# Optimization experiments

Measured on AMD Instinct MI355X. Metric: run time of the kernel, lower is better.

The kernel has to match this reference:

```python
import jax, jax.numpy as jnp
import numpy as np

B, L, D = 4, 2048, 1024
H = 16
HD = D // H  # head_dim = 64
BASE = 10000.0


def rope_cos_sin(seq_len, head_dim, dtype=jnp.float32):
    inv_freq = 1.0 / (BASE ** (jnp.arange(0, head_dim, 2, dtype=jnp.float32) / head_dim))
    t = jnp.arange(seq_len, dtype=jnp.float32)
    freqs = jnp.outer(t, inv_freq)  # [L, HD/2]
    return jnp.cos(freqs).astype(dtype), jnp.sin(freqs).astype(dtype)


def apply_rope(x, cos, sin):
    # x: [B, H, L, HD]; cos/sin: [L, HD/2]
    x1 = x[..., ::2]
    x2 = x[..., 1::2]
    c = cos[None, None, :, :]
    s = sin[None, None, :, :]
    # NOTE: original concatenates halves (does not re-interleave)
    return jnp.concatenate([x1 * c - x2 * s, x1 * s + x2 * c], axis=-1)


def setup_inputs() -> dict:
    key = jax.random.key(0)
    k1, k2, k3 = jax.random.split(key, 3)
    x = jax.random.normal(k1, (B, L, D), dtype=jnp.float32)
    W_qkv = jax.random.normal(k2, (3 * D, D), dtype=jnp.float32) * (D ** -0.5)
    W_proj = jax.random.normal(k3, (D, D), dtype=jnp.float32) * (D ** -0.5)
    return {"x": x, "W_qkv": W_qkv, "W_proj": W_proj}


def reference(x, W_qkv, W_proj):
    b, l, d = x.shape
    scale = HD ** -0.5
    qkv = jnp.einsum('bld,ed->ble', x, W_qkv)            # [B, L, 3D]
    qkv = qkv.reshape(b, l, 3, H, HD)
    q, k, v = (jnp.transpose(qkv[:, :, i], (0, 2, 1, 3)) for i in range(3))  # [B,H,L,HD]
    cos, sin = rope_cos_sin(l, HD, x.dtype)
    q = apply_rope(q, cos, sin)
    k = apply_rope(k, cos, sin)
    attn = jnp.einsum('bhqd,bhkd->bhqk', q, k) * scale   # [B,H,L,L]
    attn = jax.nn.softmax(attn, axis=-1)
    out = jnp.einsum('bhqk,bhkd->bhqd', attn, v)         # [B,H,L,HD]
    out = jnp.transpose(out, (0, 2, 1, 3)).reshape(b, l, d)
    return jnp.einsum('bld,ed->ble', out, W_proj)
```

## Files before the change

### kernel.cpp

```cpp
#include <hip/hip_runtime.h>
#include <hip/hip_bf16.h>

typedef unsigned short u16;
typedef unsigned int u32;
typedef __attribute__((ext_vector_type(8))) short bf16x8;
typedef __attribute__((ext_vector_type(4))) float f32x4;

#define NL 2048
#define NH 16

__device__ __forceinline__ float bf2f(u16 v) {
    union { float f; unsigned u; } x; x.u = ((unsigned)v) << 16; return x.f;
}
__device__ __forceinline__ u16 f2bf(float f) {
    union { __hip_bfloat16 h; u16 u; } x; x.h = __float2bfloat16(f); return x.u;
}
__device__ __forceinline__ u32 pk2(float a, float b) {
    union { float f; u32 u; } x, y; x.f = a; y.f = b;
    return ((x.u + 0x8000u) >> 16) | ((y.u + 0x8000u) & 0xffff0000u);
}
__device__ __forceinline__ u32 pkt(float lo, float hi) {
    union { float f; u32 u; } x, y; x.f = lo; y.f = hi;
    return __builtin_amdgcn_perm(y.u, x.u, 0x07060302u);
}
#if __has_builtin(__builtin_amdgcn_exp2f)
#define EXP2F(x) __builtin_amdgcn_exp2f(x)
#else
#define EXP2F(x) __expf((x) * 0.69314718056f)
#endif

__device__ __forceinline__ void gload_lds16(const u16* g, u16* l) {
    __builtin_amdgcn_global_load_lds(
        (__attribute__((address_space(1))) void*)(g),
        (__attribute__((address_space(3))) void*)(l), 16, 0, 0);
}

__global__ __launch_bounds__(256) void cast_all_k(const float* __restrict__ x,
                                                  const float* __restrict__ wq,
                                                  const float* __restrict__ wp,
                                                  u16* __restrict__ xo,
                                                  u16* __restrict__ wqo,
                                                  u16* __restrict__ wpo) {
    int i = blockIdx.x * 256 + threadIdx.x;
    const float* src; u16* dst; int off;
    if (i < 2097152)      { src = x;  dst = xo;  off = i; }
    else if (i < 2883584) { src = wq; dst = wqo; off = i - 2097152; }
    else                  { src = wp; dst = wpo; off = i - 2883584; }
    float4 v = *(const float4*)&src[(size_t)off * 4];
    u16 tmp[4] = {f2bf(v.x), f2bf(v.y), f2bf(v.z), f2bf(v.w)};
    *(ushort4*)&dst[(size_t)off * 4] = *(ushort4*)tmp;
}

__global__ __launch_bounds__(256) void rope_table_k(float* __restrict__ cosT,
                                                    float* __restrict__ sinT) {
    int idx = blockIdx.x * 256 + threadIdx.x;
    int l = idx >> 5, i = idx & 31;
    float invf = exp2f(-(float)i * 0.41524101186092029f);
    float ang = (float)l * invf;
    cosT[idx] = cosf(ang);
    sinT[idx] = sinf(ang);
}

template <typename OutT>
__global__ __launch_bounds__(256) void gemm_bt(const u16* __restrict__ A,
                                               const u16* __restrict__ Bm,
                                               OutT* __restrict__ C,
                                               int M, int N, int K) {
    __shared__ u16 As[128][64];
    __shared__ u16 Bs[128][64];
    const int t = threadIdx.x;
    const int lane = t & 63, wave = t >> 6;
    const int quad = lane >> 4, lrow = lane & 15;
    const int wr = wave >> 1, wc = wave & 1;
    const size_t m0 = (size_t)blockIdx.y * 128, n0 = (size_t)blockIdx.x * 128;

    const int srow = wave * 32 + (lane >> 3);
    const int scg  = (lane & 7) ^ (lane >> 3);

    f32x4 acc[4][4];
#pragma unroll
    for (int i = 0; i < 4; ++i)
#pragma unroll
        for (int j = 0; j < 4; ++j) acc[i][j] = (f32x4)0.0f;

    for (int k0 = 0; k0 < K; k0 += 64) {
#pragma unroll
        for (int j = 0; j < 4; ++j) {
            gload_lds16(&A[(m0 + srow + j * 8) * K + k0 + scg * 8],
                        &As[wave * 32 + j * 8][0]);
            gload_lds16(&Bm[(n0 + srow + j * 8) * K + k0 + scg * 8],
                        &Bs[wave * 32 + j * 8][0]);
        }
        __syncthreads();
#pragma unroll
        for (int ks = 0; ks < 2; ++ks) {
            bf16x8 av[4], bv[4];
#pragma unroll
            for (int i = 0; i < 4; ++i)
                av[i] = *(const bf16x8*)
                    &As[wr * 64 + i * 16 + lrow][(((ks << 2) | quad) ^ (lrow & 7)) << 3];
#pragma unroll
            for (int j = 0; j < 4; ++j)
                bv[j] = *(const bf16x8*)
                    &Bs[wc * 64 + j * 16 + lrow][(((ks << 2) | quad) ^ (lrow & 7)) << 3];
#pragma unroll
            for (int i = 0; i < 4; ++i)
#pragma unroll
                for (int j = 0; j < 4; ++j)
                    acc[i][j] = __builtin_amdgcn_mfma_f32_16x16x32_bf16(
                        av[i], bv[j], acc[i][j], 0, 0, 0);
        }
        __syncthreads();
    }
#pragma unroll
    for (int i = 0; i < 4; ++i)
#pragma unroll
        for (int r = 0; r < 4; ++r) {
            size_t row = m0 + wr * 64 + i * 16 + quad * 4 + r;
#pragma unroll
            for (int j = 0; j < 4; ++j) {
                size_t col = n0 + wc * 64 + j * 16 + lrow;
                if constexpr (sizeof(OutT) == 4)
                    C[row * N + col] = acc[i][j][r];
                else
                    C[row * N + col] = f2bf(acc[i][j][r]);
            }
        }
}

__global__ __launch_bounds__(512, 2) void gemm256_bt(const u16* __restrict__ A,
                                                     const u16* __restrict__ Bm,
                                                     u16* __restrict__ C,
                                                     int M, int N, int K) {
    __shared__ __align__(16) char smem[131072];
    const int t = threadIdx.x;
    const int lane = t & 63, w = t >> 6;
    const int quad = lane >> 4, lq = lane & 15;
    const int wm = w >> 2, wn = w & 3;
    const int rsub = lane >> 3;
    const int scg  = (lane & 7) ^ rsub;
    const size_t m0 = (size_t)blockIdx.y * 256, n0 = (size_t)blockIdx.x * 256;
    const int NT = K >> 6;

#define ASB(buf) ((u16(*)[64])(smem + (size_t)(buf) * 65536))
#define BSB(buf) ((u16(*)[64])(smem + (size_t)(buf) * 65536 + 32768))
#define STAGE_A(buf, half, kt) { \
    const size_t kro_ = (size_t)(kt) * 64 + (size_t)(scg * 8); \
    gload_lds16(&A[(m0 + (half) * 128 + w * 16 + 0 + rsub) * (size_t)K + kro_], \
                &ASB(buf)[(half) * 128 + w * 16 + 0][0]); \
    gload_lds16(&A[(m0 + (half) * 128 + w * 16 + 8 + rsub) * (size_t)K + kro_], \
                &ASB(buf)[(half) * 128 + w * 16 + 8][0]); }
#define STAGE_B(buf, half, kt) { \
    const size_t kro_ = (size_t)(kt) * 64 + (size_t)(scg * 8); \
    gload_lds16(&Bm[(n0 + (half) * 128 + w * 16 + 0 + rsub) * (size_t)K + kro_], \
                &BSB(buf)[(half) * 128 + w * 16 + 0][0]); \
    gload_lds16(&Bm[(n0 + (half) * 128 + w * 16 + 8 + rsub) * (size_t)K + kro_], \
                &BSB(buf)[(half) * 128 + w * 16 + 8][0]); }
#define RD_A(dst, rowbase) { \
    _Pragma("unroll") for (int m_ = 0; m_ < 4; ++m_) \
    _Pragma("unroll") for (int ks_ = 0; ks_ < 2; ++ks_) \
        dst[m_][ks_] = *(const bf16x8*) \
            &Ac[(rowbase) + m_ * 16 + lq][(((ks_ << 2) | quad) ^ (lq & 7)) << 3]; }
#define RD_B(dst, rowbase) { \
    _Pragma("unroll") for (int n_ = 0; n_ < 2; ++n_) \
    _Pragma("unroll") for (int ks_ = 0; ks_ < 2; ++ks_) \
        dst[n_][ks_] = *(const bf16x8*) \
            &Bc[(rowbase) + n_ * 16 + lq][(((ks_ << 2) | quad) ^ (lq & 7)) << 3]; }
#define MM(QM, QN, bvv) { \
    _Pragma("unroll") for (int m_ = 0; m_ < 4; ++m_) \
    _Pragma("unroll") for (int n_ = 0; n_ < 2; ++n_) \
    _Pragma("unroll") for (int ks_ = 0; ks_ < 2; ++ks_) \
        acc[QM][QN][m_][n_] = __builtin_amdgcn_mfma_f32_16x16x32_bf16( \
            av[m_][ks_], bvv[n_][ks_], acc[QM][QN][m_][n_], 0, 0, 0); }

    f32x4 acc[2][2][4][2];
#pragma unroll
    for (int a = 0; a < 2; ++a)
#pragma unroll
        for (int b = 0; b < 2; ++b)
#pragma unroll
            for (int m = 0; m < 4; ++m)
#pragma unroll
                for (int n = 0; n < 2; ++n) acc[a][b][m][n] = (f32x4)0.0f;
    bf16x8 av[4][2], bv0[2][2], bv1[2][2];

    STAGE_A(0, 0, 0); STAGE_B(0, 0, 0); STAGE_B(0, 1, 0); STAGE_A(0, 1, 0);
    asm volatile("s_waitcnt vmcnt(4)" ::: "memory");
    __builtin_amdgcn_s_barrier();

    for (int kt = 0; kt < NT - 1; ++kt) {
        const int cur = kt & 1, nxt = cur ^ 1;
        u16 (*Ac)[64] = ASB(cur);
        u16 (*Bc)[64] = BSB(cur);

        RD_A(av, wm * 64);
        RD_B(bv0, wn * 32);
        STAGE_A(nxt, 0, kt + 1);
        __builtin_amdgcn_s_barrier();
        __builtin_amdgcn_s_setprio(1);
        MM(0, 0, bv0);
        __builtin_amdgcn_s_setprio(0);
        asm volatile("s_waitcnt vmcnt(4)" ::: "memory");
        __builtin_amdgcn_s_barrier();

        RD_B(bv1, 128 + wn * 32);
        STAGE_B(nxt, 0, kt + 1);
        __builtin_amdgcn_s_barrier();
        __builtin_amdgcn_s_setprio(1);
        MM(0, 1, bv1);
        __builtin_amdgcn_s_setprio(0);
        asm volatile("s_waitcnt vmcnt(4)" ::: "memory");
        __builtin_amdgcn_s_barrier();

        RD_A(av, 128 + wm * 64);
        STAGE_B(nxt, 1, kt + 1);
        __builtin_amdgcn_s_barrier();
        __builtin_amdgcn_s_setprio(1);
        MM(1, 1, bv1);
        __builtin_amdgcn_s_setprio(0);
        __builtin_amdgcn_s_barrier();

        RD_B(bv0, wn * 32);
        STAGE_A(nxt, 1, kt + 1);
        __builtin_amdgcn_s_barrier();
        __builtin_amdgcn_s_setprio(1);
        MM(1, 0, bv0);
        __builtin_amdgcn_s_setprio(0);
        asm volatile("s_waitcnt vmcnt(4)" ::: "memory");
        __builtin_amdgcn_s_barrier();
    }

    {
        u16 (*Ac)[64] = ASB((NT - 1) & 1);
        u16 (*Bc)[64] = BSB((NT - 1) & 1);
        RD_A(av, wm * 64);
        RD_B(bv0, wn * 32);
        MM(0, 0, bv0);
        asm volatile("s_waitcnt vmcnt(2)" ::: "memory");
        __builtin_amdgcn_s_barrier();
        RD_B(bv1, 128 + wn * 32);
        MM(0, 1, bv1);
        asm volatile("s_waitcnt vmcnt(0)" ::: "memory");
        __builtin_amdgcn_s_barrier();
        RD_A(av, 128 + wm * 64);
        MM(1, 1, bv1);
        MM(1, 0, bv0);
    }

#pragma unroll
    for (int QM = 0; QM < 2; ++QM)
#pragma unroll
        for (int QN = 0; QN < 2; ++QN)
#pragma unroll
            for (int m = 0; m < 4; ++m)
#pragma unroll
                for (int r = 0; r < 4; ++r) {
                    size_t row = m0 + QM * 128 + wm * 64 + m * 16 + quad * 4 + r;
#pragma unroll
                    for (int n = 0; n < 2; ++n) {
                        size_t col = n0 + QN * 128 + wn * 32 + n * 16 + lq;
                        C[row * N + col] = f2bf(acc[QM][QN][m][n][r]);
                    }
                }
#undef ASB
#undef BSB
#undef STAGE_A
#undef STAGE_B
#undef RD_A
#undef RD_B
#undef MM
}

__global__ __launch_bounds__(256) void rope_vt_k(const u16* __restrict__ qkv,
                                                 const float* __restrict__ cosT,
                                                 const float* __restrict__ sinT,
                                                 u16* __restrict__ Q,
                                                 u16* __restrict__ Ko,
                                                 u16* __restrict__ VT) {
    __shared__ u16 vtile[64][72];
    const int lt = blockIdx.x, bh = blockIdx.y;
    const int b = bh >> 4, h = bh & 15;
    const int l0 = lt * 64;
    const int t = threadIdx.x;
    const float SC = 0.180336879f;
#pragma unroll
    for (int c = 0; c < 2; ++c) {
        int flat8 = c * 256 + t;
        int li = flat8 >> 3, dg = flat8 & 7;
        const u16* rowp = qkv + (size_t)(b * NL + l0 + li) * 3072 + h * 64 + dg * 8;
        uint4 qv = *(const uint4*)rowp;
        uint4 kv = *(const uint4*)(rowp + 1024);
        uint4 vv = *(const uint4*)(rowp + 2048);
        *(uint4*)&vtile[li][dg * 8] = vv;
        float4 cs = *(const float4*)&cosT[(l0 + li) * 32 + dg * 4];
        float4 sn = *(const float4*)&sinT[(l0 + li) * 32 + dg * 4];
        union { float f; u32 u; } w;
        float e0, o0, e1, o1, e2, o2, e3, o3;
        w.u = qv.x << 16; e0 = w.f; w.u = qv.x & 0xffff0000u; o0 = w.f;
        w.u = qv.y << 16; e1 = w.f; w.u = qv.y & 0xffff0000u; o1 = w.f;
        w.u = qv.z << 16; e2 = w.f; w.u = qv.z & 0xffff0000u; o2 = w.f;
        w.u = qv.w << 16; e3 = w.f; w.u = qv.w & 0xffff0000u; o3 = w.f;
        float c0 = cs.x * SC, c1 = cs.y * SC, c2 = cs.z * SC, c3 = cs.w * SC;
        float s0 = sn.x * SC, s1 = sn.y * SC, s2 = sn.z * SC, s3 = sn.w * SC;
        size_t ob = ((size_t)(b * NH + h) * NL + l0 + li) * 64;
        *(uint2*)&Q[ob + dg * 4] =
            make_uint2(pk2(e0 * c0 - o0 * s0, e1 * c1 - o1 * s1),
                       pk2(e2 * c2 - o2 * s2, e3 * c3 - o3 * s3));
        *(uint2*)&Q[ob + 32 + dg * 4] =
            make_uint2(pk2(e0 * s0 + o0 * c0, e1 * s1 + o1 * c1),
                       pk2(e2 * s2 + o2 * c2, e3 * s3 + o3 * c3));
        float f0, g0, f1, g1, f2, g2, f3, g3;
        w.u = kv.x << 16; f0 = w.f; w.u = kv.x & 0xffff0000u; g0 = w.f;
        w.u = kv.y << 16; f1 = w.f; w.u = kv.y & 0xffff0000u; g1 = w.f;
        w.u = kv.z << 16; f2 = w.f; w.u = kv.z & 0xffff0000u; g2 = w.f;
        w.u = kv.w << 16; f3 = w.f; w.u = kv.w & 0xffff0000u; g3 = w.f;
        *(uint2*)&Ko[ob + dg * 4] =
            make_uint2(pk2(f0 * cs.x - g0 * sn.x, f1 * cs.y - g1 * sn.y),
                       pk2(f2 * cs.z - g2 * sn.z, f3 * cs.w - g3 * sn.w));
        *(uint2*)&Ko[ob + 32 + dg * 4] =
            make_uint2(pk2(f0 * sn.x + g0 * cs.x, f1 * sn.y + g1 * cs.y),
                       pk2(f2 * sn.z + g2 * cs.z, f3 * sn.w + g3 * cs.w));
    }
    __syncthreads();
#pragma unroll
    for (int c = 0; c < 2; ++c) {
        int flat8 = c * 256 + t;
        int d = flat8 >> 3, lg = flat8 & 7;
        u16 tmp[8];
#pragma unroll
        for (int e = 0; e < 8; ++e) tmp[e] = vtile[lg * 8 + e][d];
        *(uint4*)&VT[((size_t)(bh * 64 + d)) * NL + l0 + lg * 8] = *(uint4*)tmp;
    }
}

__global__ __launch_bounds__(512, 4) void attn_k(const u16* __restrict__ Q,
                                                 const u16* __restrict__ Kg,
                                                 const u16* __restrict__ VT,
                                                 u16* __restrict__ Og) {
    __shared__ __align__(16) char smem[65536];
    u16 (*KsB)[64][64] = (u16(*)[64][64])(smem);
    u16 (*VsB)[64][64] = (u16(*)[64][64])(smem + 16384);
    u16* PsBase = (u16*)(smem + 32768);
    const int t = threadIdx.x;
    const int lane = t & 63, wave = t >> 6;
    const int quad = lane >> 4, lq = lane & 15;
    u16* PsW = PsBase + wave * 2048;

    const int qt = blockIdx.x, bh = blockIdx.y;
    const int q0 = qt * 256;
    const size_t qkbase = (size_t)bh * NL * 64;

    const int rsub = lane >> 3;
    const int scg  = (lane & 7) ^ rsub;

    u16 (*Qtmp)[64] = (u16(*)[64])(smem + 32768);
#pragma unroll
    for (int j = 0; j < 4; ++j)
        gload_lds16(&Q[qkbase + (size_t)(q0 + wave * 32 + j * 8 + rsub) * 64 + scg * 8],
                    &Qtmp[wave * 32 + j * 8][0]);
    const u16* kptr = Kg + qkbase + (size_t)(wave * 8 + rsub) * 64 + scg * 8;
    const u16* vptr = VT + qkbase + (size_t)(wave * 8 + rsub) * NL + scg * 8;
    gload_lds16(kptr, &KsB[0][wave * 8][0]);
    gload_lds16(vptr, &VsB[0][wave * 8][0]);
    kptr += 64 * 64;
    vptr += 64;
    __syncthreads();
    bf16x8 bq[2][2];
#pragma unroll
    for (int qh = 0; qh < 2; ++qh)
#pragma unroll
        for (int ks = 0; ks < 2; ++ks)
            bq[qh][ks] = *(const bf16x8*)
                &Qtmp[wave * 32 + qh * 16 + lq][(((ks << 2) | quad) ^ (lq & 7)) << 3];

    const bf16x8 ones = (bf16x8)(short)16256;
    f32x4 ot[2][4];
#pragma unroll
    for (int qh = 0; qh < 2; ++qh)
#pragma unroll
        for (int mt = 0; mt < 4; ++mt) ot[qh][mt] = (f32x4)0.0f;
    f32x4 lacc[2] = {(f32x4)0.0f, (f32x4)0.0f};

    for (int kc = 0; kc < NL / 64; ++kc) {
        __syncthreads();
        if (kc < NL / 64 - 1) {
            gload_lds16(kptr, &KsB[(kc + 1) & 1][wave * 8][0]);
            gload_lds16(vptr, &VsB[(kc + 1) & 1][wave * 8][0]);
            kptr += 64 * 64;
            vptr += 64;
        }
        const int cur = kc & 1;

        f32x4 st[2][4];
#pragma unroll
        for (int qh = 0; qh < 2; ++qh)
#pragma unroll
            for (int mt = 0; mt < 4; ++mt) st[qh][mt] = (f32x4)0.0f;
#pragma unroll
        for (int ks = 0; ks < 2; ++ks)
#pragma unroll
            for (int mt = 0; mt < 4; ++mt) {
                bf16x8 ak = *(const bf16x8*)
                    &KsB[cur][mt * 16 + lq][(((ks << 2) | quad) ^ (lq & 7)) << 3];
                st[0][mt] = __builtin_amdgcn_mfma_f32_16x16x32_bf16(ak, bq[0][ks], st[0][mt], 0, 0, 0);
                st[1][mt] = __builtin_amdgcn_mfma_f32_16x16x32_bf16(ak, bq[1][ks], st[1][mt], 0, 0, 0);
            }

#pragma unroll
        for (int qh = 0; qh < 2; ++qh)
#pragma unroll
            for (int mt = 0; mt < 4; ++mt) {
                int pblk = (mt * 2 + (quad >> 1)) ^ (lq & 7);
                *(uint2*)&PsW[(qh * 16 + lq) * 64 + pblk * 8 + (quad & 1) * 4] =
                    make_uint2(pkt(EXP2F(st[qh][mt][0]), EXP2F(st[qh][mt][1])),
                               pkt(EXP2F(st[qh][mt][2]), EXP2F(st[qh][mt][3])));
            }
        __builtin_amdgcn_s_waitcnt(0xc07f);

#pragma unroll
        for (int ks = 0; ks < 2; ++ks) {
            const int sw = (((ks << 2) | quad) ^ (lq & 7)) * 8;
            bf16x8 bp0 = *(const bf16x8*)&PsW[lq * 64 + sw];
            bf16x8 bp1 = *(const bf16x8*)&PsW[(16 + lq) * 64 + sw];
            lacc[0] = __builtin_amdgcn_mfma_f32_16x16x32_bf16(ones, bp0, lacc[0], 0, 0, 0);
            lacc[1] = __builtin_amdgcn_mfma_f32_16x16x32_bf16(ones, bp1, lacc[1], 0, 0, 0);
#pragma unroll
            for (int mt = 0; mt < 4; ++mt) {
                bf16x8 av = *(const bf16x8*)
                    &VsB[cur][mt * 16 + lq][(((ks << 2) | quad) ^ (lq & 7)) << 3];
                ot[0][mt] = __builtin_amdgcn_mfma_f32_16x16x32_bf16(av, bp0, ot[0][mt], 0, 0, 0);
                ot[1][mt] = __builtin_amdgcn_mfma_f32_16x16x32_bf16(av, bp1, ot[1][mt], 0, 0, 0);
            }
        }
    }

    __syncthreads();
    float* OT_ls = (float*)(smem + wave * 4352);
    float* Ls_ls = (float*)(smem + 34816);
    const int b = bh >> 4, h = bh & 15;
    const int qq = lane >> 2, dblk = lane & 3;
#pragma unroll
    for (int qh = 0; qh < 2; ++qh) {
#pragma unroll
        for (int mt = 0; mt < 4; ++mt)
#pragma unroll
            for (int r = 0; r < 4; ++r)
                OT_ls[(mt * 16 + quad * 4 + r) * 17 + lq] = ot[qh][mt][r];
        if (quad == 0) Ls_ls[wave * 16 + lq] = lacc[qh][0];
        __builtin_amdgcn_s_waitcnt(0xc07f);

        float rls = 1.0f / Ls_ls[wave * 16 + qq];
        u16 tmp[16];
#pragma unroll
        for (int e = 0; e < 16; ++e)
            tmp[e] = f2bf(OT_ls[(dblk * 16 + e) * 17 + qq] * rls);
        size_t orow = (size_t)b * NL + q0 + wave * 32 + qh * 16 + qq;
        size_t obase = orow * 1024 + h * 64 + dblk * 16;
        *(uint4*)&Og[obase] = *(uint4*)&tmp[0];
        *(uint4*)&Og[obase + 8] = *(uint4*)&tmp[8];
    }
}

extern "C" void kernel_launch(void* const* d_in, const int* in_sizes, int n_in,
                              void* d_out, int out_size, void* d_ws, size_t ws_size,
                              hipStream_t stream) {
    const float* x     = (const float*)d_in[0];
    const float* Wqkv  = (const float*)d_in[1];
    const float* Wproj = (const float*)d_in[2];
    float* out = (float*)d_out;

    char* ws = (char*)d_ws;
    u16* qkv     = (u16*)ws;
    u16* attnout = (u16*)ws;
    u16* Qw      = (u16*)(ws + 50331648);
    u16* Kw      = (u16*)(ws + 67108864);
    u16* VTw     = (u16*)(ws + 83886080);
    float* cosT  = (float*)(ws + 100663296);
    float* sinT  = (float*)(ws + 100925440);
    u16* x_bf    = (u16*)(ws + 101187584);
    u16* Wqkv_bf = (u16*)(ws + 117964800);
    u16* Wproj_bf= (u16*)(ws + 124256256);

    rope_table_k<<<256, 256, 0, stream>>>(cosT, sinT);
    cast_all_k<<<12288, 256, 0, stream>>>(x, Wqkv, Wproj, x_bf, Wqkv_bf, Wproj_bf);
    gemm256_bt<<<dim3(12, 32), 512, 0, stream>>>(x_bf, Wqkv_bf, qkv, 8192, 3072, 1024);
    rope_vt_k<<<dim3(32, 64), 256, 0, stream>>>(qkv, cosT, sinT, Qw, Kw, VTw);
    attn_k<<<dim3(8, 64), 512, 0, stream>>>(Qw, Kw, VTw, attnout);
    gemm_bt<float><<<dim3(8, 64), 256, 0, stream>>>(attnout, Wproj_bf, out, 8192, 1024, 1024);
}
```

Baseline: 265.7 us.

## Keep softmax P in registers via permlane swaps and remap block order

Replaces the per-wave LDS round-trip for the exponentiated score tile P with cross-lane permlane32/permlane16 swaps. These rearrange the MFMA accumulator layout directly into the B-operand layout for the PV matmul. This removes LDS writes, a waitcnt and LDS reads per key chunk. The block index is also remapped so that consecutive workgroups cover eight heads of the same query tile, which changes L2 locality. The risk is a lane-mapping error in the swap, and the remap assumes the grid is 8 by 64.

```diff
diff --git a/kernel.cpp b/kernel.cpp
--- a/kernel.cpp
+++ b/kernel.cpp
@@ -5,6 +5,7 @@
 typedef unsigned int u32;
 typedef __attribute__((ext_vector_type(8))) short bf16x8;
 typedef __attribute__((ext_vector_type(4))) float f32x4;
+typedef __attribute__((ext_vector_type(2))) unsigned int u32x2;
 
 #define NL 2048
 #define NH 16
@@ -28,6 +29,21 @@
 #else
 #define EXP2F(x) __expf((x) * 0.69314718056f)
 #endif
+
+__device__ __forceinline__ void quad_xchg(u32& a, u32& b) {
+#if __has_builtin(__builtin_amdgcn_permlane32_swap) && __has_builtin(__builtin_amdgcn_permlane16_swap)
+    u32x2 r0 = __builtin_amdgcn_permlane32_swap(a, b, false, false);
+    u32x2 r1 = __builtin_amdgcn_permlane16_swap(r0.x, r0.y, false, false);
+    a = r1.x; b = r1.y;
+#else
+    asm volatile("s_nop 1\n\t"
+                 "v_permlane32_swap_b32 %0, %1\n\t"
+                 "s_nop 1\n\t"
+                 "v_permlane16_swap_b32 %0, %1\n\t"
+                 "s_nop 1"
+                 : "+v"(a), "+v"(b));
+#endif
+}
 
 __device__ __forceinline__ void gload_lds16(const u16* g, u16* l) {
     __builtin_amdgcn_global_load_lds(
@@ -340,13 +356,13 @@
     __shared__ __align__(16) char smem[65536];
     u16 (*KsB)[64][64] = (u16(*)[64][64])(smem);
     u16 (*VsB)[64][64] = (u16(*)[64][64])(smem + 16384);
-    u16* PsBase = (u16*)(smem + 32768);
     const int t = threadIdx.x;
     const int lane = t & 63, wave = t >> 6;
     const int quad = lane >> 4, lq = lane & 15;
-    u16* PsW = PsBase + wave * 2048;
-
-    const int qt = blockIdx.x, bh = blockIdx.y;
+
+    const int flat = blockIdx.y * 8 + blockIdx.x;
+    const int qt = (flat >> 3) & 7;
+    const int bh = (flat & 7) + ((flat >> 6) << 3);
     const int q0 = qt * 256;
     const size_t qkbase = (size_t)bh * NL * 64;
 
@@ -406,30 +422,44 @@
                 st[1][mt] = __builtin_amdgcn_mfma_f32_16x16x32_bf16(ak, bq[1][ks], st[1][mt], 0, 0, 0);
             }
 
-#pragma unroll
-        for (int qh = 0; qh < 2; ++qh)
+        bf16x8 bp[2][2];
+#pragma unroll
+        for (int qh = 0; qh < 2; ++qh) {
+            u32 w0[4], w1[4];
 #pragma unroll
             for (int mt = 0; mt < 4; ++mt) {
-                int pblk = (mt * 2 + (quad >> 1)) ^ (lq & 7);
-                *(uint2*)&PsW[(qh * 16 + lq) * 64 + pblk * 8 + (quad & 1) * 4] =
-                    make_uint2(pkt(EXP2F(st[qh][mt][0]), EXP2F(st[qh][mt][1])),
-                               pkt(EXP2F(st[qh][mt][2]), EXP2F(st[qh][mt][3])));
+                float p0 = EXP2F(st[qh][mt][0]);
+                float p1 = EXP2F(st[qh][mt][1]);
+                float p2 = EXP2F(st[qh][mt][2]);
+                float p3 = EXP2F(st[qh][mt][3]);
+                w0[mt] = pkt(p0, p1);
+                w1[mt] = pkt(p2, p3);
             }
-        __builtin_amdgcn_s_waitcnt(0xc07f);
+#pragma unroll
+            for (int ks = 0; ks < 2; ++ks) {
+                u32 a0 = w0[2 * ks], b0 = w0[2 * ks + 1];
+                u32 a1 = w1[2 * ks], b1 = w1[2 * ks + 1];
+                quad_xchg(a0, b0);
+                quad_xchg(a1, b1);
+                union { u32 u[4]; bf16x8 v; } bb;
+                bb.u[0] = a0;
+                bb.u[1] = a1;
+                bb.u[2] = b0;
+                bb.u[3] = b1;
+                bp[qh][ks] = bb.v;
+            }
+        }
 
 #pragma unroll
         for (int ks = 0; ks < 2; ++ks) {
-            const int sw = (((ks << 2) | quad) ^ (lq & 7)) * 8;
-            bf16x8 bp0 = *(const bf16x8*)&PsW[lq * 64 + sw];
-            bf16x8 bp1 = *(const bf16x8*)&PsW[(16 + lq) * 64 + sw];
-            lacc[0] = __builtin_amdgcn_mfma_f32_16x16x32_bf16(ones, bp0, lacc[0], 0, 0, 0);
-            lacc[1] = __builtin_amdgcn_mfma_f32_16x16x32_bf16(ones, bp1, lacc[1], 0, 0, 0);
+            lacc[0] = __builtin_amdgcn_mfma_f32_16x16x32_bf16(ones, bp[0][ks], lacc[0], 0, 0, 0);
+            lacc[1] = __builtin_amdgcn_mfma_f32_16x16x32_bf16(ones, bp[1][ks], lacc[1], 0, 0, 0);
 #pragma unroll
             for (int mt = 0; mt < 4; ++mt) {
                 bf16x8 av = *(const bf16x8*)
                     &VsB[cur][mt * 16 + lq][(((ks << 2) | quad) ^ (lq & 7)) << 3];
-                ot[0][mt] = __builtin_amdgcn_mfma_f32_16x16x32_bf16(av, bp0, ot[0][mt], 0, 0, 0);
-                ot[1][mt] = __builtin_amdgcn_mfma_f32_16x16x32_bf16(av, bp1, ot[1][mt], 0, 0, 0);
+                ot[0][mt] = __builtin_amdgcn_mfma_f32_16x16x32_bf16(av, bp[0][ks], ot[0][mt], 0, 0, 0);
+                ot[1][mt] = __builtin_amdgcn_mfma_f32_16x16x32_bf16(av, bp[1][ks], ot[1][mt], 0, 0, 0);
             }
         }
     }
```

After: 263.7 us. Within noise of the previous version (-0.8%).
